# Performance work log

Measured on AMD Instinct MI355X. Metric: run time of the kernel, lower is better.

Reference implementation:

```python
import jax, jax.numpy as jnp
import numpy as np

B, S, H, NH, NE = 4, 1024, 256, 4, 4
D = H // NH  # head_unit = 64
EPS = 1e-8


def layernorm(x, g, b):
    m = jnp.mean(x, axis=-1, keepdims=True)
    v = jnp.mean((x - m) ** 2, axis=-1, keepdims=True)
    return (x - m) / jnp.sqrt(v + EPS) * g + b


def setup_inputs() -> dict:
    key = jax.random.key(0)
    ks = jax.random.split(key, 18)
    sc = 0.05
    return {
        "x": jax.random.normal(ks[0], (B, S, H), jnp.float32),
        # MoEMultiHead params
        "hl_w": jax.random.normal(ks[1], (NH, D, H), jnp.float32) * sc,   # head_layer weights (out,in)
        "hl_b": jax.random.normal(ks[2], (NH, D), jnp.float32) * sc,
        "wq": jax.random.normal(ks[3], (NH, NE, D, D), jnp.float32) * sc,  # w_q[i*NH+j] -> wq[i,j]
        "wk": jax.random.normal(ks[4], (NH, D, D), jnp.float32) * sc,
        "wv": jax.random.normal(ks[5], (NH, D, D), jnp.float32) * sc,
        "gate_w": jax.random.normal(ks[6], (NH, NE, NE * D), jnp.float32) * sc,
        "gate_b": jax.random.normal(ks[7], (NH, NE), jnp.float32) * sc,
        "ln_g": jnp.ones((D,), jnp.float32),
        "ln_b": jnp.zeros((D,), jnp.float32),
        # FFN params (built inside forward in torch; materialized here)
        "fc1_w": jax.random.normal(ks[8], (D, D), jnp.float32) * sc,
        "fc1_b": jax.random.normal(ks[9], (D,), jnp.float32) * sc,
        "fc2_w": jax.random.normal(ks[10], (D, D), jnp.float32) * sc,
        "fc2_b": jax.random.normal(ks[11], (D,), jnp.float32) * sc,
        "fnorm_g": jnp.ones((D,), jnp.float32),
        "fnorm_b": jnp.zeros((D,), jnp.float32),
        "fgate_w": jax.random.normal(ks[12], (NH, H), jnp.float32) * sc,
    }


def reference(x, hl_w, hl_b, wq, wk, wv, gate_w, gate_b, ln_g, ln_b,
              fc1_w, fc1_b, fc2_w, fc2_b, fnorm_g, fnorm_b, fgate_w):
    b, s, h = x.shape
    nh, d, _ = wk.shape
    ne = wq.shape[1]
    # per-head projection of full hidden -> head_unit  (B, NH, S, D)
    sx = jnp.einsum('bsh,ndh->bnsd', x, hl_w) + hl_b[None, :, None, :]
    pad = sx == 0  # padding mask, same for all experts
    # per-(head, expert) q; per-head k, v
    q = jnp.einsum('bnsd,neod->bneso', sx, wq)       # (B,NH,NE,S,D)
    k = jnp.einsum('bnsd,nod->bnso', sx, wk)         # (B,NH,S,D)
    v = jnp.einsum('bnsd,nod->bnso', sx, wv)
    causal = jnp.where(jnp.tril(jnp.ones((s, s), bool)), 0.0, -jnp.inf).astype(x.dtype)
    # NOTE: original MULTIPLIES by sqrt(head_unit) (bug-faithful)
    scores = jnp.einsum('bnesd,bntd->bnest', q, k) * (d ** 0.5) + causal
    att = jax.nn.softmax(scores, axis=-1)
    qkv = jnp.einsum('bnest,bntd->bnesd', att, v)
    qkv = jnp.where(pad[:, :, None], 0.0, qkv)
    # concat experts along feature dim: (B,NH,S,NE*D)
    out = jnp.transpose(qkv, (0, 1, 3, 2, 4)).reshape(b, nh, s, ne * d)
    gs = jax.nn.softmax(jnp.einsum('bnsf,nef->bnse', out, gate_w) + gate_b[None, :, None, :], axis=-1)
    mixed = jnp.einsum('bnsed,bnse->bnsd', out.reshape(b, nh, s, ne, d), gs)
    # bug-faithful residual: split_x[i] indexes the BATCH dim with head index i
    resid = sx[jnp.arange(nh), jnp.arange(nh)]  # (NH, S, D), broadcast over batch
    hn = layernorm(mixed + resid, ln_g, ln_b)   # (B,NH,S,D); dropout inactive (p=0)
    f_n = jnp.transpose(hn, (0, 2, 1, 3)).reshape(b, s, h)
    # ---- FFN (fresh module in torch; deterministic params here) ----
    fx = f_n.reshape(b, s, nh, d)  # torch.split along feature dim
    pm = fx == 0
    hx = jnp.where(pm, 0.0, fx @ fc1_w.T + fc1_b)
    hx = jax.nn.relu(hx)
    hx = jnp.where(pm, 0.0, hx @ fc2_w.T + fc2_b)
    hx = layernorm(hx + fx, fnorm_g, fnorm_b)
    fout = hx.reshape(b, s, h)
    fg = jax.nn.softmax(fout @ fgate_w.T, axis=-1)  # (B,S,NH)
    return (fout.reshape(b, s, nh, d) * fg[..., None]).reshape(b, s, h)
```

## Files before the change

### kernel.cpp

```cpp
#include <hip/hip_runtime.h>
#include <math.h>

typedef unsigned short u16;
typedef __attribute__((ext_vector_type(8))) unsigned short us8;
typedef __attribute__((ext_vector_type(4))) unsigned short us4;
typedef __attribute__((ext_vector_type(8))) short bf16x8;
typedef __attribute__((ext_vector_type(4))) float f32x4;

constexpr int B_ = 4, S_ = 1024, H_ = 256, NH_ = 4, NE_ = 4, D_ = 64;
constexpr float EPS_ = 1e-8f;

__device__ __forceinline__ u16 f2bf(float f){
  unsigned u = __float_as_uint(f);
  unsigned rnd = 0x7fffu + ((u>>16)&1u);
  return (u16)((u + rnd)>>16);
}
__device__ __forceinline__ float bf2f(u16 u){ return __uint_as_float(((unsigned)u)<<16); }
__device__ __forceinline__ us4 pack4(float4 a){
  us4 r; r[0]=f2bf(a.x); r[1]=f2bf(a.y); r[2]=f2bf(a.z); r[3]=f2bf(a.w);
  return r;
}
__device__ __forceinline__ unsigned cvtpk(float lo, float hi){
  unsigned r;
  asm("v_cvt_pk_bf16_f32 %0, %1, %2" : "=v"(r) : "v"(lo), "v"(hi));
  return r;
}
#define MFMA16(a,b,c) __builtin_amdgcn_mfma_f32_16x16x32_bf16((bf16x8)(a),(bf16x8)(b),(c),0,0,0)

__global__ __launch_bounds__(256) void k_sx(const float* __restrict__ x, const float* __restrict__ hlw,
                                            const float* __restrict__ hlb,
                                            float* __restrict__ sx, u16* __restrict__ sxb){
  int mt = blockIdx.x >> 3, nt = blockIdx.x & 7;
  int tid = threadIdx.x, w = tid>>6, l = tid&63, lr = l>>4, lc = l&15;
  __shared__ u16 Xs[64*64];
  __shared__ u16 Ws[32*64];
  const int swl = (lc&7)<<3;
  f32x4 acc[2] = {{0,0,0,0},{0,0,0,0}};
  for(int ks=0; ks<4; ++ks){
    __syncthreads();
    #pragma unroll
    for(int it=0; it<4; ++it){
      int g = tid + it*256; int row = g>>4, c4 = (g&15)*4;
      float4 a = *(const float4*)(x + ((size_t)(mt*64+row))*H_ + ks*64 + c4);
      *(us4*)&Xs[row*64 + (c4 ^ ((row&7)<<3))] = pack4(a);
    }
    #pragma unroll
    for(int it=0; it<2; ++it){
      int g = tid + it*256; int row = g>>4, c4 = (g&15)*4;
      float4 a = *(const float4*)(hlw + ((size_t)(nt*32+row))*H_ + ks*64 + c4);
      *(us4*)&Ws[row*64 + (c4 ^ ((row&7)<<3))] = pack4(a);
    }
    __syncthreads();
    bf16x8 a0 = *(const bf16x8*)&Xs[(w*16+lc)*64 + ((lr*8   ) ^ swl)];
    bf16x8 a1 = *(const bf16x8*)&Xs[(w*16+lc)*64 + ((lr*8+32) ^ swl)];
    #pragma unroll
    for(int j=0;j<2;j++){
      const u16* wr = &Ws[(j*16+lc)*64];
      bf16x8 b0 = *(const bf16x8*)(wr + ((lr*8   ) ^ swl));
      bf16x8 b1 = *(const bf16x8*)(wr + ((lr*8+32) ^ swl));
      acc[j] = MFMA16(a0,b0,acc[j]);
      acc[j] = MFMA16(a1,b1,acc[j]);
    }
  }
  #pragma unroll
  for(int j=0;j<2;j++){
    int col = nt*32 + j*16 + lc;
    int n = col>>6, d = col&63;
    float bias = hlb[col];
    #pragma unroll
    for(int r=0;r<4;r++){
      int m = mt*64 + w*16 + lr*4 + r;
      int b = m>>10, s = m&1023;
      float v = acc[j][r] + bias;
      size_t idx = ((size_t)(b*NH_+n)*S_+s)*D_ + d;
      sx[idx] = v; sxb[idx] = f2bf(v);
    }
  }
}

__global__ __launch_bounds__(256) void k_qkv(const u16* __restrict__ sxb, const float* __restrict__ wq,
            const float* __restrict__ wk, const float* __restrict__ wv,
            u16* __restrict__ qb, u16* __restrict__ kbf, u16* __restrict__ vbT){
  int bid = blockIdx.x;
  int half = bid&1, mt = (bid>>1)&63, n = bid>>7;
  int tid = threadIdx.x, w = tid>>6, l = tid&63, lr = l>>4, lc = l&15;
  __shared__ u16 As[64*64];
  __shared__ u16 Ws[192*64];
  const int swl = (lc&7)<<3;
  int b = (mt*64)>>10, s0 = (mt*64)&1023;
  { int sr = tid>>3, sc = (tid&7)*8, sw = (sr&7)<<3;
    const u16* base = sxb + ((size_t)(b*NH_+n)*S_ + s0)*D_;
    *(us8*)&As[ sr     *64 + (sc ^ sw)] = *(const us8*)(base + (size_t) sr    *D_ + sc);
    *(us8*)&As[(sr+32)*64 + (sc ^ sw)] = *(const us8*)(base + (size_t)(sr+32)*D_ + sc);
  }
  #pragma unroll
  for(int it=0; it<12; ++it){
    int g = tid + it*256; int row = g>>4, c4 = (g&15)*4;
    int o = half*192 + row;
    const float* src;
    if(o < 256)      src = wq + ((size_t)((n*NE_ + (o>>6))*D_ + (o&63)))*D_;
    else if(o < 320) src = wk + ((size_t)(n*D_ + (o-256)))*D_;
    else             src = wv + ((size_t)(n*D_ + (o-320)))*D_;
    float4 a = *(const float4*)(src + c4);
    *(us4*)&Ws[row*64 + (c4 ^ ((row&7)<<3))] = pack4(a);
  }
  __syncthreads();
  bf16x8 a0 = *(const bf16x8*)&As[(w*16+lc)*64 + ((lr*8   ) ^ swl)];
  bf16x8 a1 = *(const bf16x8*)&As[(w*16+lc)*64 + ((lr*8+32) ^ swl)];
  f32x4 acc[12];
  #pragma unroll
  for(int j=0;j<12;j++) acc[j] = (f32x4){0,0,0,0};
  #pragma unroll
  for(int j=0;j<12;j++){
    const u16* wr = &Ws[(j*16+lc)*64];
    bf16x8 b0 = *(const bf16x8*)(wr + ((lr*8   ) ^ swl));
    bf16x8 b1 = *(const bf16x8*)(wr + ((lr*8+32) ^ swl));
    acc[j] = MFMA16(a0,b0,acc[j]);
    acc[j] = MFMA16(a1,b1,acc[j]);
  }
  #pragma unroll
  for(int j=0;j<12;j++){
    int o = half*192 + j*16 + lc;
    #pragma unroll
    for(int r=0;r<4;r++){
      int s = s0 + w*16 + lr*4 + r;
      float v = acc[j][r];
      if(o < 256){
        int e = o>>6, d = o&63;
        qb[((size_t)((b*NH_+n)*NE_+e)*S_ + s)*D_ + d] = f2bf(v*11.5415603f);
      } else if(o < 320){
        kbf[((size_t)(b*NH_+n)*S_ + s)*D_ + (o-256)] = f2bf(v);
      } else {
        int d = o-320;
        vbT[((size_t)(b*NH_+n)*D_ + d)*S_ + s] = f2bf(v);
      }
    }
  }
}

__global__ __launch_bounds__(256,4) void k_attn(const u16* __restrict__ qb, const u16* __restrict__ kb,
        const u16* __restrict__ vbT, const u16* __restrict__ sxb, u16* __restrict__ attoutb){
  int bid = blockIdx.x;
  int head = bid & 63, idx = bid >> 6;
  int g = idx>>2, pos = idx&3;
  int qt = (g&1) ? (15 - (g>>1) - 2*pos) : ((g>>1) + 2*pos);
  int bq = head>>2, e = head&3;
  int tid = threadIdx.x, w = tid>>6, l = tid&63, lr = l>>4, lc = l&15;
  __shared__ u16 Ks[2][64*64];
  __shared__ u16 VT[2][64*64];
  __shared__ u16 Pb[4][16*64];
  const u16* kh = kb  + (size_t)bq*S_*D_;
  const u16* vh = vbT + (size_t)bq*D_*S_;
  const int swl = (lc&7)<<3;
  const int sr = tid>>3, sc = (tid&7)*8, sw = (sr&7)<<3;

  const u16* qrow = qb + ((size_t)head*S_ + qt*64 + w*16 + lc)*D_;
  bf16x8 qf0 = *(const bf16x8*)(qrow + lr*8);
  bf16x8 qf1 = *(const bf16x8*)(qrow + lr*8 + 32);
  f32x4 Oa[4];
  #pragma unroll
  for(int j=0;j<4;j++) Oa[j] = (f32x4){0,0,0,0};
  float l_i = 0.f;

  us8 rg[4];
  {
    rg[0] = *(const us8*)(kh + (size_t) sr    *D_ + sc);
    rg[1] = *(const us8*)(kh + (size_t)(sr+32)*D_ + sc);
    rg[2] = *(const us8*)(vh + (size_t) sr    *S_ + sc);
    rg[3] = *(const us8*)(vh + (size_t)(sr+32)*S_ + sc);
    *(us8*)&Ks[0][ sr    *64 + (sc ^ sw)] = rg[0];
    *(us8*)&Ks[0][(sr+32)*64 + (sc ^ sw)] = rg[1];
    *(us8*)&VT[0][ sr    *64 + (sc ^ sw)] = rg[2];
    *(us8*)&VT[0][(sr+32)*64 + (sc ^ sw)] = rg[3];
  }
  for(int kt=0; kt<=qt; ++kt){
    int cur = kt&1;
    __syncthreads();
    bool more = kt < qt;
    if(more){
      rg[0] = *(const us8*)(kh + ((size_t)(kt+1)*64 +  sr    )*D_ + sc);
      rg[1] = *(const us8*)(kh + ((size_t)(kt+1)*64 + (sr+32))*D_ + sc);
      rg[2] = *(const us8*)(vh + (size_t) sr    *S_ + (kt+1)*64 + sc);
      rg[3] = *(const us8*)(vh + (size_t)(sr+32)*S_ + (kt+1)*64 + sc);
    }
    f32x4 Sa[4];
    __builtin_amdgcn_s_setprio(1);
    #pragma unroll
    for(int j=0;j<4;j++){
      const u16* kr = &Ks[cur][(j*16+lc)*64];
      bf16x8 a0 = *(const bf16x8*)(kr + ((lr*8   ) ^ swl));
      bf16x8 a1 = *(const bf16x8*)(kr + ((lr*8+32) ^ swl));
      f32x4 z = (f32x4){0,0,0,0};
      z = MFMA16(a0,qf0,z);
      z = MFMA16(a1,qf1,z);
      Sa[j] = z;
    }
    __builtin_amdgcn_s_setprio(0);
    if(kt==qt){
      int q = w*16 + lc;
      #pragma unroll
      for(int j=0;j<4;j++)
        #pragma unroll
        for(int r=0;r<4;r++)
          if(j*16 + lr*4 + r > q) Sa[j][r] = -INFINITY;
    }
    #pragma unroll
    for(int j=0;j<4;j++)
      #pragma unroll
      for(int r=0;r<4;r++) Sa[j][r] = exp2f(Sa[j][r] - 20.f);
    float rs0 = (Sa[0][0]+Sa[0][1]) + (Sa[0][2]+Sa[0][3]);
    float rs1 = (Sa[1][0]+Sa[1][1]) + (Sa[1][2]+Sa[1][3]);
    float rs2 = (Sa[2][0]+Sa[2][1]) + (Sa[2][2]+Sa[2][3]);
    float rs3 = (Sa[3][0]+Sa[3][1]) + (Sa[3][2]+Sa[3][3]);
    l_i += (rs0+rs1) + (rs2+rs3);
    #pragma unroll
    for(int j=0;j<4;j++){
      uint2 pp;
      pp.x = cvtpk(Sa[j][0], Sa[j][1]);
      pp.y = cvtpk(Sa[j][2], Sa[j][3]);
      *(uint2*)&Pb[w][lc*64 + ((j*16+lr*4) ^ swl)] = pp;
    }
    asm volatile("s_waitcnt lgkmcnt(0)" ::: "memory");
    bf16x8 pB0 = *(const bf16x8*)&Pb[w][lc*64 + ((lr*8   ) ^ swl)];
    bf16x8 pB1 = *(const bf16x8*)&Pb[w][lc*64 + ((lr*8+32) ^ swl)];
    __builtin_amdgcn_s_setprio(1);
    #pragma unroll
    for(int jd=0;jd<4;jd++){
      const u16* vr = &VT[cur][(jd*16+lc)*64];
      bf16x8 v0 = *(const bf16x8*)(vr + ((lr*8   ) ^ swl));
      bf16x8 v1 = *(const bf16x8*)(vr + ((lr*8+32) ^ swl));
      Oa[jd] = MFMA16(v0,pB0,Oa[jd]);
      Oa[jd] = MFMA16(v1,pB1,Oa[jd]);
    }
    __builtin_amdgcn_s_setprio(0);
    if(more){
      int nb = cur^1;
      *(us8*)&Ks[nb][ sr    *64 + (sc ^ sw)] = rg[0];
      *(us8*)&Ks[nb][(sr+32)*64 + (sc ^ sw)] = rg[1];
      *(us8*)&VT[nb][ sr    *64 + (sc ^ sw)] = rg[2];
      *(us8*)&VT[nb][(sr+32)*64 + (sc ^ sw)] = rg[3];
    }
  }
  l_i += __shfl_xor(l_i,16);
  l_i += __shfl_xor(l_i,32);
  int qg = qt*64 + w*16 + lc;
  float inv = 1.f/l_i;
  const u16* sxp = sxb + ((size_t)bq*S_ + qg)*D_;
  u16* op = attoutb + ((size_t)bq*S_ + qg)*(NE_*D_) + e*D_;
  #pragma unroll
  for(int jd=0;jd<4;jd++){
    int d0 = jd*16 + lr*4;
    us4 sxv = *(const us4*)(sxp + d0);
    us4 ov;
    #pragma unroll
    for(int r=0;r<4;r++){
      float o = Oa[jd][r]*inv;
      ov[r] = ((sxv[r]&0x7fff)==0) ? (u16)0 : f2bf(o);
    }
    *(us4*)(op + d0) = ov;
  }
}

__global__ __launch_bounds__(256) void k_tail(const u16* __restrict__ attoutb, const float* __restrict__ gw,
      const float* __restrict__ gb, const float* __restrict__ sx,
      const float* __restrict__ lng, const float* __restrict__ lnb,
      const float* __restrict__ w1g, const float* __restrict__ b1g,
      const float* __restrict__ w2g, const float* __restrict__ b2g,
      const float* __restrict__ fng, const float* __restrict__ fnb,
      const float* __restrict__ fgw, float* __restrict__ out){
  int bid = blockIdx.x;
  int gs0 = bid*16, b = gs0>>10, s0 = gs0&1023;
  int tid = threadIdx.x;
  int row = tid>>4, l16 = tid&15;
  int w = tid>>6, l = tid&63, lr = l>>4, lc = l&15;
  __shared__ float Fx[64][64];
  __shared__ u16 FnB[64*64];
  __shared__ u16 W1[64*64], W2[64*64], H1[64*64];
  __shared__ float Red[4][16][4];

  #pragma unroll
  for(int g2=0; g2<2; ++g2){
    int g = tid*2+g2; int r2 = g>>3, c0 = (g&7)*8;
    float4 a = *(const float4*)(w1g + r2*64 + c0), bb = *(const float4*)(w1g + r2*64 + c0 + 4);
    us8 p;
    p[0]=f2bf(a.x);p[1]=f2bf(a.y);p[2]=f2bf(a.z);p[3]=f2bf(a.w);
    p[4]=f2bf(bb.x);p[5]=f2bf(bb.y);p[6]=f2bf(bb.z);p[7]=f2bf(bb.w);
    *(us8*)&W1[r2*64 + (c0 ^ ((r2&7)<<3))] = p;
    a = *(const float4*)(w2g + r2*64 + c0); bb = *(const float4*)(w2g + r2*64 + c0 + 4);
    p[0]=f2bf(a.x);p[1]=f2bf(a.y);p[2]=f2bf(a.z);p[3]=f2bf(a.w);
    p[4]=f2bf(bb.x);p[5]=f2bf(bb.y);p[6]=f2bf(bb.z);p[7]=f2bf(bb.w);
    *(us8*)&W2[r2*64 + (c0 ^ ((r2&7)<<3))] = p;
  }
  const int d0 = l16*4;
  for(int n=0;n<NH_;++n){
    f32x4 o[4];
    const u16* ar = attoutb + ((size_t)(b*NH_+n)*S_ + s0 + row)*(NE_*D_);
    #pragma unroll
    for(int e=0;e<4;e++){
      us4 t = *(const us4*)(ar + e*64 + d0);
      #pragma unroll
      for(int k=0;k<4;k++) o[e][k] = bf2f(t[k]);
    }
    float lg4[4];
    #pragma unroll
    for(int eg=0; eg<4; ++eg){
      const float* gr = gw + (size_t)(n*NE_+eg)*(NE_*D_);
      float p = 0.f;
      #pragma unroll
      for(int e=0;e<4;e++){
        f32x4 g4 = *(const f32x4*)(gr + e*64 + d0);
        p += o[e][0]*g4[0] + o[e][1]*g4[1] + o[e][2]*g4[2] + o[e][3]*g4[3];
      }
      #pragma unroll
      for(int off=1; off<16; off<<=1) p += __shfl_xor(p, off);
      lg4[eg] = p + gb[n*NE_+eg];
    }
    float mx = fmaxf(fmaxf(lg4[0],lg4[1]),fmaxf(lg4[2],lg4[3]));
    float se = 0.f;
    #pragma unroll
    for(int eg=0;eg<4;eg++){ lg4[eg]=__expf(lg4[eg]-mx); se+=lg4[eg]; }
    float inv = 1.f/se;
    f32x4 res = *(const f32x4*)(sx + ((size_t)(n*NH_+n)*S_ + s0 + row)*D_ + d0);
    float tv[4];
    #pragma unroll
    for(int k=0;k<4;k++){
      float mixk = o[0][k]*lg4[0] + o[1][k]*lg4[1] + o[2][k]*lg4[2] + o[3][k]*lg4[3];
      tv[k] = mixk*inv + res[k];
    }
    float sum = tv[0]+tv[1]+tv[2]+tv[3];
    #pragma unroll
    for(int off=1; off<16; off<<=1) sum += __shfl_xor(sum, off);
    float mean = sum*(1.f/64.f);
    float vs = 0.f;
    #pragma unroll
    for(int k=0;k<4;k++){ float d = tv[k]-mean; vs += d*d; }
    #pragma unroll
    for(int off=1; off<16; off<<=1) vs += __shfl_xor(vs, off);
    float rstd = rsqrtf(vs*(1.f/64.f)+EPS_);
    f32x4 lgv = *(const f32x4*)(lng + d0);
    f32x4 lbv = *(const f32x4*)(lnb + d0);
    int hr = n*16+row;
    us4 pk;
    f32x4 yv;
    #pragma unroll
    for(int k=0;k<4;k++){
      float y = (tv[k]-mean)*rstd*lgv[k] + lbv[k];
      yv[k] = y; pk[k] = f2bf(y);
    }
    *(f32x4*)&Fx[hr][d0] = yv;
    *(us4*)&FnB[hr*64 + (d0 ^ ((hr&7)<<3))] = pk;
  }
  __syncthreads();
  const int swl = (lc&7)<<3;
  bf16x8 a0 = *(const bf16x8*)&FnB[(w*16+lc)*64 + ((lr*8   ) ^ swl)];
  bf16x8 a1 = *(const bf16x8*)&FnB[(w*16+lc)*64 + ((lr*8+32) ^ swl)];
  f32x4 acc1[4];
  #pragma unroll
  for(int jn=0;jn<4;jn++) acc1[jn] = (f32x4){0,0,0,0};
  #pragma unroll
  for(int jn=0;jn<4;jn++){
    const u16* wr = &W1[(jn*16+lc)*64];
    bf16x8 b0 = *(const bf16x8*)(wr + ((lr*8   ) ^ swl));
    bf16x8 b1 = *(const bf16x8*)(wr + ((lr*8+32) ^ swl));
    acc1[jn] = MFMA16(a0,b0,acc1[jn]);
    acc1[jn] = MFMA16(a1,b1,acc1[jn]);
  }
  #pragma unroll
  for(int jn=0;jn<4;jn++){
    int dout = jn*16+lc;
    float bias = b1g[dout];
    #pragma unroll
    for(int rr=0;rr<4;rr++){
      int hr = w*16 + lr*4 + rr;
      float v = acc1[jn][rr] + bias;
      v = (Fx[hr][dout]==0.f) ? 0.f : v;
      v = fmaxf(v, 0.f);
      H1[hr*64 + (dout ^ ((hr&7)<<3))] = f2bf(v);
    }
  }
  __syncthreads();
  a0 = *(const bf16x8*)&H1[(w*16+lc)*64 + ((lr*8   ) ^ swl)];
  a1 = *(const bf16x8*)&H1[(w*16+lc)*64 + ((lr*8+32) ^ swl)];
  f32x4 acc2[4];
  #pragma unroll
  for(int jn=0;jn<4;jn++) acc2[jn] = (f32x4){0,0,0,0};
  #pragma unroll
  for(int jn=0;jn<4;jn++){
    const u16* wr = &W2[(jn*16+lc)*64];
    bf16x8 b0 = *(const bf16x8*)(wr + ((lr*8   ) ^ swl));
    bf16x8 b1 = *(const bf16x8*)(wr + ((lr*8+32) ^ swl));
    acc2[jn] = MFMA16(a0,b0,acc2[jn]);
    acc2[jn] = MFMA16(a1,b1,acc2[jn]);
  }
  float tv2[4][4];
  #pragma unroll
  for(int jn=0;jn<4;jn++){
    int dout = jn*16+lc;
    float bias = b2g[dout];
    #pragma unroll
    for(int rr=0;rr<4;rr++){
      int hr = w*16 + lr*4 + rr;
      float fx = Fx[hr][dout];
      float v = acc2[jn][rr] + bias;
      v = (fx==0.f) ? 0.f : v;
      tv2[jn][rr] = v + fx;
    }
  }
  float sum_r[4], vs_r[4];
  #pragma unroll
  for(int rr=0;rr<4;rr++) sum_r[rr] = tv2[0][rr]+tv2[1][rr]+tv2[2][rr]+tv2[3][rr];
  #pragma unroll
  for(int off=1; off<16; off<<=1)
    #pragma unroll
    for(int rr=0;rr<4;rr++) sum_r[rr] += __shfl_xor(sum_r[rr], off);
  float mean_r[4];
  #pragma unroll
  for(int rr=0;rr<4;rr++) mean_r[rr] = sum_r[rr]*(1.f/64.f);
  #pragma unroll
  for(int rr=0;rr<4;rr++){
    float a = tv2[0][rr]-mean_r[rr], b2v = tv2[1][rr]-mean_r[rr];
    float c = tv2[2][rr]-mean_r[rr], d = tv2[3][rr]-mean_r[rr];
    vs_r[rr] = a*a + b2v*b2v + c*c + d*d;
  }
  #pragma unroll
  for(int off=1; off<16; off<<=1)
    #pragma unroll
    for(int rr=0;rr<4;rr++) vs_r[rr] += __shfl_xor(vs_r[rr], off);
  float y2[4][4];
  #pragma unroll
  for(int jn=0;jn<4;jn++){
    int dout = jn*16+lc;
    float g = fng[dout], bb = fnb[dout];
    #pragma unroll
    for(int rr=0;rr<4;rr++){
      float rstd = rsqrtf(vs_r[rr]*(1.f/64.f)+EPS_);
      y2[jn][rr] = (tv2[jn][rr]-mean_r[rr])*rstd*g + bb;
    }
  }
  float fg4[4][4];
  #pragma unroll
  for(int j=0;j<4;j++)
    #pragma unroll
    for(int jn=0;jn<4;jn++)
      fg4[j][jn] = fgw[(size_t)j*H_ + w*64 + jn*16 + lc];
  float pj[4][4];
  #pragma unroll
  for(int j=0;j<4;j++)
    #pragma unroll
    for(int rr=0;rr<4;rr++)
      pj[j][rr] = y2[0][rr]*fg4[j][0] + y2[1][rr]*fg4[j][1] + y2[2][rr]*fg4[j][2] + y2[3][rr]*fg4[j][3];
  #pragma unroll
  for(int off=1; off<16; off<<=1)
    #pragma unroll
    for(int j=0;j<4;j++)
      #pragma unroll
      for(int rr=0;rr<4;rr++) pj[j][rr] += __shfl_xor(pj[j][rr], off);
  if(lc==0){
    #pragma unroll
    for(int rr=0;rr<4;rr++)
      #pragma unroll
      for(int j=0;j<4;j++) Red[w][lr*4+rr][j] = pj[j][rr];
  }
  __syncthreads();
  #pragma unroll
  for(int rr=0;rr<4;rr++){
    int srow = lr*4+rr;
    float lgf[4];
    #pragma unroll
    for(int j=0;j<4;j++) lgf[j] = Red[0][srow][j]+Red[1][srow][j]+Red[2][srow][j]+Red[3][srow][j];
    float mx2 = fmaxf(fmaxf(lgf[0],lgf[1]),fmaxf(lgf[2],lgf[3]));
    float se2 = 0.f;
    #pragma unroll
    for(int j=0;j<4;j++){ lgf[j]=__expf(lgf[j]-mx2); se2+=lgf[j]; }
    float gsn = lgf[w]/se2;
    float* op = out + ((size_t)(gs0 + srow))*H_ + w*64;
    #pragma unroll
    for(int jn=0;jn<4;jn++) op[jn*16+lc] = y2[jn][rr]*gsn;
  }
}

extern "C" void kernel_launch(void* const* d_in, const int* in_sizes, int n_in,
                              void* d_out, int out_size, void* d_ws, size_t ws_size,
                              hipStream_t stream){
  const float* x      = (const float*)d_in[0];
  const float* hl_w   = (const float*)d_in[1];
  const float* hl_b   = (const float*)d_in[2];
  const float* wq     = (const float*)d_in[3];
  const float* wk     = (const float*)d_in[4];
  const float* wv     = (const float*)d_in[5];
  const float* gate_w = (const float*)d_in[6];
  const float* gate_b = (const float*)d_in[7];
  const float* ln_g   = (const float*)d_in[8];
  const float* ln_b   = (const float*)d_in[9];
  const float* fc1_w  = (const float*)d_in[10];
  const float* fc1_b  = (const float*)d_in[11];
  const float* fc2_w  = (const float*)d_in[12];
  const float* fc2_b  = (const float*)d_in[13];
  const float* fnorm_g= (const float*)d_in[14];
  const float* fnorm_b= (const float*)d_in[15];
  const float* fgate_w= (const float*)d_in[16];

  const size_t NSD = (size_t)B_*NH_*S_*D_;
  float* ws      = (float*)d_ws;
  float* sx      = ws;
  u16*   sxb     = (u16*)(sx + NSD);
  u16*   attoutb = sxb + NSD;
  u16*   qb      = attoutb + NSD*NE_;
  u16*   kbf     = qb + NSD*NE_;
  u16*   vbT     = kbf + NSD;

  k_sx  <<<512,  256, 0, stream>>>(x, hl_w, hl_b, sx, sxb);
  k_qkv <<<512,  256, 0, stream>>>(sxb, wq, wk, wv, qb, kbf, vbT);
  k_attn<<<1024, 256, 0, stream>>>(qb, kbf, vbT, sxb, attoutb);
  k_tail<<<256,  256, 0, stream>>>(attoutb, gate_w, gate_b, sx, ln_g, ln_b,
                                   fc1_w, fc1_b, fc2_w, fc2_b,
                                   fnorm_g, fnorm_b, fgate_w, (float*)d_out);
}
```

Before: 61.95 us.

## Widen k_sx tiles to full heads and restructure k_tail head-parallel mixing

k_sx now computes 64-column tiles, one full head per block, with half as many blocks. This halves redundant loads and bf16 conversions of x and simplifies the output indexing. In k_tail, each wavefront now handles one head, with 4 lanes per row holding 16 features each, replacing the serial loop over heads. This cuts the shuffle reductions from 4 steps to 2 and removes the per-head serialization, but uses more registers per thread. Fx gets padded rows to reduce LDS bank conflicts.

```diff
diff --git a/kernel.cpp b/kernel.cpp
--- a/kernel.cpp
+++ b/kernel.cpp
@@ -30,12 +30,12 @@
 __global__ __launch_bounds__(256) void k_sx(const float* __restrict__ x, const float* __restrict__ hlw,
                                             const float* __restrict__ hlb,
                                             float* __restrict__ sx, u16* __restrict__ sxb){
-  int mt = blockIdx.x >> 3, nt = blockIdx.x & 7;
+  int mt = blockIdx.x >> 2, nt = blockIdx.x & 3;
   int tid = threadIdx.x, w = tid>>6, l = tid&63, lr = l>>4, lc = l&15;
   __shared__ u16 Xs[64*64];
-  __shared__ u16 Ws[32*64];
+  __shared__ u16 Ws[64*64];
   const int swl = (lc&7)<<3;
-  f32x4 acc[2] = {{0,0,0,0},{0,0,0,0}};
+  f32x4 acc[4] = {{0,0,0,0},{0,0,0,0},{0,0,0,0},{0,0,0,0}};
   for(int ks=0; ks<4; ++ks){
     __syncthreads();
     #pragma unroll
@@ -45,16 +45,16 @@
       *(us4*)&Xs[row*64 + (c4 ^ ((row&7)<<3))] = pack4(a);
     }
     #pragma unroll
-    for(int it=0; it<2; ++it){
+    for(int it=0; it<4; ++it){
       int g = tid + it*256; int row = g>>4, c4 = (g&15)*4;
-      float4 a = *(const float4*)(hlw + ((size_t)(nt*32+row))*H_ + ks*64 + c4);
+      float4 a = *(const float4*)(hlw + ((size_t)(nt*64+row))*H_ + ks*64 + c4);
       *(us4*)&Ws[row*64 + (c4 ^ ((row&7)<<3))] = pack4(a);
     }
     __syncthreads();
     bf16x8 a0 = *(const bf16x8*)&Xs[(w*16+lc)*64 + ((lr*8   ) ^ swl)];
     bf16x8 a1 = *(const bf16x8*)&Xs[(w*16+lc)*64 + ((lr*8+32) ^ swl)];
     #pragma unroll
-    for(int j=0;j<2;j++){
+    for(int j=0;j<4;j++){
       const u16* wr = &Ws[(j*16+lc)*64];
       bf16x8 b0 = *(const bf16x8*)(wr + ((lr*8   ) ^ swl));
       bf16x8 b1 = *(const bf16x8*)(wr + ((lr*8+32) ^ swl));
@@ -63,16 +63,15 @@
     }
   }
   #pragma unroll
-  for(int j=0;j<2;j++){
-    int col = nt*32 + j*16 + lc;
-    int n = col>>6, d = col&63;
-    float bias = hlb[col];
+  for(int j=0;j<4;j++){
+    int d = j*16 + lc;
+    float bias = hlb[nt*64 + d];
     #pragma unroll
     for(int r=0;r<4;r++){
       int m = mt*64 + w*16 + lr*4 + r;
       int b = m>>10, s = m&1023;
       float v = acc[j][r] + bias;
-      size_t idx = ((size_t)(b*NH_+n)*S_+s)*D_ + d;
+      size_t idx = ((size_t)(b*NH_+nt)*S_+s)*D_ + d;
       sx[idx] = v; sxb[idx] = f2bf(v);
     }
   }
@@ -271,9 +270,8 @@
   int bid = blockIdx.x;
   int gs0 = bid*16, b = gs0>>10, s0 = gs0&1023;
   int tid = threadIdx.x;
-  int row = tid>>4, l16 = tid&15;
   int w = tid>>6, l = tid&63, lr = l>>4, lc = l&15;
-  __shared__ float Fx[64][64];
+  __shared__ float Fx[64][68];
   __shared__ u16 FnB[64*64];
   __shared__ u16 W1[64*64], W2[64*64], H1[64*64];
   __shared__ float Red[4][16][4];
@@ -291,64 +289,80 @@
     p[4]=f2bf(bb.x);p[5]=f2bf(bb.y);p[6]=f2bf(bb.z);p[7]=f2bf(bb.w);
     *(us8*)&W2[r2*64 + (c0 ^ ((r2&7)<<3))] = p;
   }
-  const int d0 = l16*4;
-  for(int n=0;n<NH_;++n){
-    f32x4 o[4];
-    const u16* ar = attoutb + ((size_t)(b*NH_+n)*S_ + s0 + row)*(NE_*D_);
-    #pragma unroll
-    for(int e=0;e<4;e++){
-      us4 t = *(const us4*)(ar + e*64 + d0);
-      #pragma unroll
-      for(int k=0;k<4;k++) o[e][k] = bf2f(t[k]);
-    }
+  {
+    int nA = tid>>6, lA = tid&63, rowA = lA>>2, lq = lA&3;
+    int dbA = lq*16;
+    const u16* ar = attoutb + ((size_t)(b*NH_+nA)*S_ + s0 + rowA)*(NE_*D_);
+    f32x4 o[4][4];
+    #pragma unroll
+    for(int e=0;e<4;e++)
+      #pragma unroll
+      for(int k4=0;k4<4;k4++){
+        us4 t = *(const us4*)(ar + e*64 + dbA + k4*4);
+        #pragma unroll
+        for(int i=0;i<4;i++) o[e][k4][i] = bf2f(t[i]);
+      }
     float lg4[4];
     #pragma unroll
     for(int eg=0; eg<4; ++eg){
-      const float* gr = gw + (size_t)(n*NE_+eg)*(NE_*D_);
+      const float* gr = gw + (size_t)(nA*NE_+eg)*(NE_*D_);
       float p = 0.f;
       #pragma unroll
-      for(int e=0;e<4;e++){
-        f32x4 g4 = *(const f32x4*)(gr + e*64 + d0);
-        p += o[e][0]*g4[0] + o[e][1]*g4[1] + o[e][2]*g4[2] + o[e][3]*g4[3];
-      }
-      #pragma unroll
-      for(int off=1; off<16; off<<=1) p += __shfl_xor(p, off);
-      lg4[eg] = p + gb[n*NE_+eg];
+      for(int e=0;e<4;e++)
+        #pragma unroll
+        for(int k4=0;k4<4;k4++){
+          f32x4 g4 = *(const f32x4*)(gr + e*64 + dbA + k4*4);
+          p += o[e][k4][0]*g4[0] + o[e][k4][1]*g4[1] + o[e][k4][2]*g4[2] + o[e][k4][3]*g4[3];
+        }
+      p += __shfl_xor(p,1);
+      p += __shfl_xor(p,2);
+      lg4[eg] = p + gb[nA*NE_+eg];
     }
     float mx = fmaxf(fmaxf(lg4[0],lg4[1]),fmaxf(lg4[2],lg4[3]));
     float se = 0.f;
     #pragma unroll
     for(int eg=0;eg<4;eg++){ lg4[eg]=__expf(lg4[eg]-mx); se+=lg4[eg]; }
     float inv = 1.f/se;
-    f32x4 res = *(const f32x4*)(sx + ((size_t)(n*NH_+n)*S_ + s0 + row)*D_ + d0);
-    float tv[4];
-    #pragma unroll
-    for(int k=0;k<4;k++){
-      float mixk = o[0][k]*lg4[0] + o[1][k]*lg4[1] + o[2][k]*lg4[2] + o[3][k]*lg4[3];
-      tv[k] = mixk*inv + res[k];
-    }
-    float sum = tv[0]+tv[1]+tv[2]+tv[3];
-    #pragma unroll
-    for(int off=1; off<16; off<<=1) sum += __shfl_xor(sum, off);
+    #pragma unroll
+    for(int eg=0;eg<4;eg++) lg4[eg] *= inv;
+    const float* rp = sx + ((size_t)(nA*NH_+nA)*S_ + s0 + rowA)*D_ + dbA;
+    f32x4 tv[4];
+    float sum = 0.f;
+    #pragma unroll
+    for(int k4=0;k4<4;k4++){
+      f32x4 res = *(const f32x4*)(rp + k4*4);
+      #pragma unroll
+      for(int i=0;i<4;i++){
+        float m2 = o[0][k4][i]*lg4[0] + o[1][k4][i]*lg4[1] + o[2][k4][i]*lg4[2] + o[3][k4][i]*lg4[3];
+        tv[k4][i] = m2 + res[i];
+        sum += tv[k4][i];
+      }
+    }
+    sum += __shfl_xor(sum,1);
+    sum += __shfl_xor(sum,2);
     float mean = sum*(1.f/64.f);
     float vs = 0.f;
     #pragma unroll
-    for(int k=0;k<4;k++){ float d = tv[k]-mean; vs += d*d; }
-    #pragma unroll
-    for(int off=1; off<16; off<<=1) vs += __shfl_xor(vs, off);
+    for(int k4=0;k4<4;k4++)
+      #pragma unroll
+      for(int i=0;i<4;i++){ float d2 = tv[k4][i]-mean; vs += d2*d2; }
+    vs += __shfl_xor(vs,1);
+    vs += __shfl_xor(vs,2);
     float rstd = rsqrtf(vs*(1.f/64.f)+EPS_);
-    f32x4 lgv = *(const f32x4*)(lng + d0);
-    f32x4 lbv = *(const f32x4*)(lnb + d0);
-    int hr = n*16+row;
-    us4 pk;
-    f32x4 yv;
-    #pragma unroll
-    for(int k=0;k<4;k++){
-      float y = (tv[k]-mean)*rstd*lgv[k] + lbv[k];
-      yv[k] = y; pk[k] = f2bf(y);
-    }
-    *(f32x4*)&Fx[hr][d0] = yv;
-    *(us4*)&FnB[hr*64 + (d0 ^ ((hr&7)<<3))] = pk;
+    int hr = nA*16+rowA;
+    #pragma unroll
+    for(int k4=0;k4<4;k4++){
+      f32x4 lgv = *(const f32x4*)(lng + dbA + k4*4);
+      f32x4 lbv = *(const f32x4*)(lnb + dbA + k4*4);
+      f32x4 yv; us4 pk;
+      #pragma unroll
+      for(int i=0;i<4;i++){
+        float y = (tv[k4][i]-mean)*rstd*lgv[i] + lbv[i];
+        yv[i]=y; pk[i]=f2bf(y);
+      }
+      *(f32x4*)&Fx[hr][dbA + k4*4] = yv;
+      *(us4*)&FnB[hr*64 + ((dbA + k4*4) ^ ((hr&7)<<3))] = pk;
+    }
   }
   __syncthreads();
   const int swl = (lc&7)<<3;
@@ -509,7 +523,7 @@
   u16*   kbf     = qb + NSD*NE_;
   u16*   vbT     = kbf + NSD;
 
-  k_sx  <<<512,  256, 0, stream>>>(x, hl_w, hl_b, sx, sxb);
+  k_sx  <<<256,  256, 0, stream>>>(x, hl_w, hl_b, sx, sxb);
   k_qkv <<<512,  256, 0, stream>>>(sxb, wq, wk, wv, qb, kbf, vbT);
   k_attn<<<1024, 256, 0, stream>>>(qb, kbf, vbT, sxb, attoutb);
   k_tail<<<256,  256, 0, stream>>>(attoutb, gate_w, gate_b, sx, ln_g, ln_b,
```

After: 64.45 us. 4.0% more time.
